# Optimization experiments

Measured on AMD Instinct MI355X. Metric: run time of the kernel, lower is better.

## Reference

```python
import jax, jax.numpy as jnp
import numpy as np

B, S, E, H, N, M, V = 8, 64, 64, 8, 2, 2, 50257
F = E  # outTrans FF hidden == embedding_size (4th ctor arg)


def setup_inputs() -> dict:
    key = jax.random.key(0)
    ks = jax.random.split(key, 10)
    sc = float(1.0 / np.sqrt(E))
    return {
        "noise": jax.random.uniform(ks[0], (B, S), jnp.float32),
        "lin_W": jax.random.normal(ks[1], (M, S, S), jnp.float32) * float(1.0 / np.sqrt(S)),
        "lin_b": jnp.zeros((M, S), jnp.float32),
        "sa_W": jax.random.normal(ks[2], (N, 4, E, E), jnp.float32) * sc,  # q,k,v,o
        "sa_b": jnp.zeros((N, 4, E), jnp.float32),
        "ca_W": jax.random.normal(ks[3], (N, 4, E, E), jnp.float32) * sc,
        "ca_b": jnp.zeros((N, 4, E), jnp.float32),
        "ff_W1": jax.random.normal(ks[4], (N, E, F), jnp.float32) * sc,
        "ff_b1": jnp.zeros((N, F), jnp.float32),
        "ff_W2": jax.random.normal(ks[5], (N, F, E), jnp.float32) * float(1.0 / np.sqrt(F)),
        "ff_b2": jnp.zeros((N, E), jnp.float32),
        "ln_g": jnp.ones((N, 3, E), jnp.float32),
        "ln_b": jnp.zeros((N, 3, E), jnp.float32),
        "emb": jax.random.normal(ks[6], (V, E), jnp.float32),
        "soft_W": jax.random.normal(ks[7], (E, V), jnp.float32) * sc,
        "soft_b": jnp.zeros((V,), jnp.float32),
        "start_id": 0,
    }


def _layernorm(x, g, b):
    m = jnp.mean(x, -1, keepdims=True)
    v = jnp.var(x, -1, keepdims=True)
    return (x - m) * jax.lax.rsqrt(v + 1e-5) * g + b


def _mha(qx, kvx, key_mask, W, bias):
    # W: [4,E,E] = (q,k,v,out). key_mask: [S] bool, True = valid key position.
    Bq, Sq, Eq = qx.shape
    d = Eq // H
    q = (qx @ W[0] + bias[0]).reshape(Bq, Sq, H, d)
    k = (kvx @ W[1] + bias[1]).reshape(Bq, -1, H, d)
    v = (kvx @ W[2] + bias[2]).reshape(Bq, -1, H, d)
    s = jnp.einsum('bqhd,bkhd->bhqk', q, k) / np.float32(np.sqrt(d))
    s = jnp.where(key_mask[None, None, None, :], s, jnp.float32(-1e9))
    a = jax.nn.softmax(s, axis=-1)
    o = jnp.einsum('bhqk,bkhd->bqhd', a, v).reshape(Bq, Sq, Eq)
    return o @ W[3] + bias[3]


def _pos_enc():
    pos = jnp.arange(S, dtype=jnp.float32)[:, None]
    i = jnp.arange(0, E, 2, dtype=jnp.float32)[None, :]
    ang = pos / jnp.power(jnp.float32(10000.0), i / E)
    pe = jnp.zeros((S, E), jnp.float32)
    return pe.at[:, 0::2].set(jnp.sin(ang)).at[:, 1::2].set(jnp.cos(ang))


def _forward(noise, lin_W, lin_b, sa_W, sa_b, ca_W, ca_b, ff_W1, ff_b1,
             ff_W2, ff_b2, ln_g, ln_b, emb, soft_W, soft_b, start_id):
    # inEmb2: M stacked Linear(S,S) on the noise
    w = noise
    for m in range(M):
        w = w @ lin_W[m] + lin_b[m]
    # unsqueeze(-1).repeat -> [B,S,S]; feature dim S == E
    w = jnp.repeat(w[:, :, None], S, axis=2)
    pe = _pos_enc()  # dropout p=0.1 is identity (module calls eval())
    Y0 = jnp.zeros((B, S, E), jnp.float32).at[:, 0].set(emb[start_id] + pe[0])

    def step(Y, tok):
        # Original re-runs all blocks on Y[:, :tok] each step (no KV cache).
        # We keep a fixed [B,S,E] buffer and mask keys >= tok: masked softmax
        # gives math identical to the truncated computation at valid positions.
        key_mask = jnp.arange(S) < tok
        out = Y
        for n in range(N):
            h = _mha(out, out, key_mask, sa_W[n], sa_b[n])
            out = _layernorm(out + h, ln_g[n, 0], ln_b[n, 0])
            h = _mha(out, w, key_mask, ca_W[n], ca_b[n])
            out = _layernorm(out + h, ln_g[n, 1], ln_b[n, 1])
            h = jax.nn.relu(out @ ff_W1[n] + ff_b1[n]) @ ff_W2[n] + ff_b2[n]
            out = _layernorm(out + h, ln_g[n, 2], ln_b[n, 2])
        tok_feat = out[:, tok - 1]                              # [B,E]
        probs = jax.nn.softmax(tok_feat @ soft_W + soft_b, -1)  # [B,V]
        nxt = jnp.argmax(probs, axis=-1)                        # greedy token
        Y = Y.at[:, tok].set(emb[nxt] + pe[tok])
        return Y, probs

    _, probs = jax.lax.scan(step, Y0, jnp.arange(1, S))
    return jnp.transpose(probs, (1, 0, 2))  # [B, S-1, V]


def reference(noise, lin_W, lin_b, sa_W, sa_b, ca_W, ca_b, ff_W1, ff_b1,
              ff_W2, ff_b2, ln_g, ln_b, emb, soft_W, soft_b, start_id):
    return _forward(noise, lin_W, lin_b, sa_W, sa_b, ca_W, ca_b, ff_W1, ff_b1,
                    ff_W2, ff_b2, ln_g, ln_b, emb, soft_W, soft_b, start_id)
```

## Files before the change

### kernel.cpp

```cpp
#include <hip/hip_runtime.h>
#include <math.h>

#define Vc 50257
#define NEG_INF (-__builtin_inff())
#define VCOLS 512
#define NVB 99
#define NB  8

#define WS_PE    0
#define WS_WV    4096
#define WS_CS    4608
#define WS_TOKF  4864
#define WS_MS    5376
#define WS_X2    5632
#define WS_SM    8192
#define WS_SS    9216
#define WS_SI    10240
#define WS_X1    16384
#define WS_Q1    49152
#define WS_K1    81920
#define WS_V1    114688
#define WS_K2G   147456
#define WS_V2G   180224


__device__ __forceinline__ float wsum64(float v) {
#pragma unroll
  for (int m = 32; m >= 1; m >>= 1) v += __shfl_xor(v, m, 64);
  return v;
}

__device__ __forceinline__ float red8(float v) {
  v += __shfl_xor(v, 1, 64);
  v += __shfl_xor(v, 2, 64);
  v += __shfl_xor(v, 4, 64);
  return v;
}

__device__ __forceinline__ float proj_lds(float xv, float* xb,
                                          const float* W,
                                          const float* __restrict__ bias, int lane) {
  xb[lane] = xv;
  asm volatile("s_waitcnt lgkmcnt(0)" ::: "memory");
  float acc = bias[lane];
  const float4* x4 = (const float4*)xb;
#pragma unroll
  for (int i = 0; i < 16; ++i) {
    float4 xc = x4[i];
    acc = fmaf(xc.x, W[(4 * i + 0) * 64 + lane], acc);
    acc = fmaf(xc.y, W[(4 * i + 1) * 64 + lane], acc);
    acc = fmaf(xc.z, W[(4 * i + 2) * 64 + lane], acc);
    acc = fmaf(xc.w, W[(4 * i + 3) * 64 + lane], acc);
  }
  asm volatile("" ::: "memory");
  return acc;
}

__device__ __forceinline__ float ln64(float xv, const float* __restrict__ g,
                                      const float* __restrict__ b, int lane) {
  float mean = wsum64(xv) * 0.015625f;
  float d = xv - mean;
  float var = wsum64(d * d) * 0.015625f;
  float r = 1.0f / sqrtf(var + 1e-5f);
  return d * r * g[lane] + b[lane];
}

struct LayerR {
  const float *saW3, *sab3, *caW0, *cab0, *caW3, *cab3,
              *ffW1, *ffb1, *ffW2, *ffb2, *g0, *be0, *g1, *be1, *g2, *be2;
  float cs1_r, cs2_r, cab1_r, cab2_r;
};

__device__ __forceinline__ void build_layer_s(LayerR& L, int n, int lane,
    const float* sWl, const float* sa_b, const float* ca_b,
    const float* ff_W1, const float* ff_b1, const float* ff_W2, const float* ff_b2,
    const float* ln_g, const float* ln_b, const float* cs_g) {
  L.saW3 = sWl;              L.sab3 = sa_b + (n * 4 + 3) * 64;
  L.caW0 = sWl + 4096;       L.cab0 = ca_b + (n * 4 + 0) * 64;
  L.caW3 = sWl + 2 * 4096;   L.cab3 = ca_b + (n * 4 + 3) * 64;
  L.ffW1 = ff_W1 + n * 4096; L.ffb1 = ff_b1 + n * 64;
  L.ffW2 = ff_W2 + n * 4096; L.ffb2 = ff_b2 + n * 64;
  L.g0 = ln_g + (n * 3 + 0) * 64;  L.be0 = ln_b + (n * 3 + 0) * 64;
  L.g1 = ln_g + (n * 3 + 1) * 64;  L.be1 = ln_b + (n * 3 + 1) * 64;
  L.g2 = ln_g + (n * 3 + 2) * 64;  L.be2 = ln_b + (n * 3 + 2) * 64;
  L.cab1_r = ca_b[(n * 4 + 1) * 64 + lane];
  L.cab2_r = ca_b[(n * 4 + 2) * 64 + lane];
  L.cs1_r = cs_g[(n * 2 + 0) * 64 + lane];
  L.cs2_r = cs_g[(n * 2 + 1) * 64 + lane];
}

__device__ float transformer_row(int lane, int t, float x, float q,
                                 const float* Kb, const float* Vb,
                                 const float* wv, float* xb, float* pb,
                                 const LayerR& P) {
  const float ISQ8 = 0.35355339059327373f;
  xb[lane] = q;
  asm volatile("s_waitcnt lgkmcnt(0)" ::: "memory");
  float a[8] = {0.f, 0.f, 0.f, 0.f, 0.f, 0.f, 0.f, 0.f};
  const float* Krow = Kb + lane * 65;
  const float4* xq4 = (const float4*)xb;
#pragma unroll
  for (int i = 0; i < 16; ++i) {
    float4 xc = xq4[i];
    a[i >> 1] = fmaf(xc.x, Krow[4 * i + 0], a[i >> 1]);
    a[i >> 1] = fmaf(xc.y, Krow[4 * i + 1], a[i >> 1]);
    a[i >> 1] = fmaf(xc.z, Krow[4 * i + 2], a[i >> 1]);
    a[i >> 1] = fmaf(xc.w, Krow[4 * i + 3], a[i >> 1]);
  }
  const bool act = lane < t;
  float m[8];
#pragma unroll
  for (int h = 0; h < 8; ++h) { a[h] = act ? a[h] * ISQ8 : NEG_INF; m[h] = a[h]; }
#pragma unroll
  for (int msk = 1; msk < 64; msk <<= 1) {
#pragma unroll
    for (int h = 0; h < 8; ++h) m[h] = fmaxf(m[h], __shfl_xor(m[h], msk, 64));
  }
  float l[8];
#pragma unroll
  for (int h = 0; h < 8; ++h) { a[h] = act ? expf(a[h] - m[h]) : 0.f; l[h] = a[h]; }
#pragma unroll
  for (int msk = 1; msk < 64; msk <<= 1) {
#pragma unroll
    for (int h = 0; h < 8; ++h) l[h] += __shfl_xor(l[h], msk, 64);
  }
#pragma unroll
  for (int h = 0; h < 8; ++h) pb[h * 64 + lane] = a[h] / l[h];
  asm volatile("s_waitcnt lgkmcnt(0)" ::: "memory");
  const float* pr = pb + (lane >> 3) * 64;
  float attn = 0.f;
  for (int k = 0; k < t; ++k) attn = fmaf(pr[k], Vb[k * 65 + lane], attn);

  float y1 = ln64(x + proj_lds(attn, xb, P.saW3, P.sab3, lane), P.g0, P.be0, lane);
  float qc = proj_lds(y1, xb, P.caW0, P.cab0, lane);
  float pa = red8(qc * P.cs1_r);
  float pc = red8(qc * P.cab1_r);
  const float4* wv4 = (const float4*)wv;
  float mc = NEG_INF;
#pragma unroll
  for (int i = 0; i < 16; ++i) {
    float4 wq = wv4[i];
    int k = 4 * i;
    if (k + 0 < t) mc = fmaxf(mc, fmaf(pa, wq.x, pc));
    if (k + 1 < t) mc = fmaxf(mc, fmaf(pa, wq.y, pc));
    if (k + 2 < t) mc = fmaxf(mc, fmaf(pa, wq.z, pc));
    if (k + 3 < t) mc = fmaxf(mc, fmaf(pa, wq.w, pc));
  }
  float lc = 0.f, z = 0.f;
#pragma unroll
  for (int i = 0; i < 16; ++i) {
    float4 wq = wv4[i];
    int k = 4 * i;
    float wk[4] = {wq.x, wq.y, wq.z, wq.w};
#pragma unroll
    for (int j = 0; j < 4; ++j) {
      if (k + j < t) {
        float raw = fmaf(pa, wk[j], pc);
        float pw = expf((raw - mc) * ISQ8);
        lc += pw;
        z = fmaf(pw, wk[j], z);
      }
    }
  }
  float oc = fmaf(z / lc, P.cs2_r, P.cab2_r);
  float y2 = ln64(y1 + proj_lds(oc, xb, P.caW3, P.cab3, lane), P.g1, P.be1, lane);
  float f = fmaxf(proj_lds(y2, xb, P.ffW1, P.ffb1, lane), 0.f);
  float y3 = ln64(y2 + proj_lds(f, xb, P.ffW2, P.ffb2, lane), P.g2, P.be2, lane);
  return y3;
}

__global__ __launch_bounds__(1024) void init_kernel(
    const float* __restrict__ noise, const float* __restrict__ lin_W,
    const float* __restrict__ lin_b, const float* __restrict__ sa_W,
    const float* __restrict__ sa_b, const float* __restrict__ ca_W,
    const float* __restrict__ emb, const int* __restrict__ start_id,
    float* __restrict__ wsf) {
  const int tid = threadIdx.x, lane = tid & 63, wvid = tid >> 6;
  __shared__ float xbuf[16 * 64];
  float* myxb = xbuf + wvid * 64;

  for (int i = tid; i < 62 * 64; i += 1024) {
    int t = 1 + (i >> 6), e = i & 63;
    double ang = (double)t / pow(10000.0, (double)(e & 62) / 64.0);
    wsf[WS_PE + t * 64 + e] = (e & 1) ? (float)cos(ang) : (float)sin(ang);
  }
  if (wvid < 8) {
    int b = wvid;
    float nz = noise[b * 64 + lane];
    float t1 = proj_lds(nz, myxb, lin_W, lin_b, lane);
    wsf[WS_WV + b * 64 + lane] = proj_lds(t1, myxb, lin_W + 4096, lin_b + 64, lane);
  } else if (wvid < 12) {
    int w = wvid - 8, n = w >> 1, which = w & 1;
    float c = 0.f;
    for (int e = 0; e < 64; ++e) c += ca_W[(n * 4 + 1 + which) * 4096 + e * 64 + lane];
    wsf[WS_CS + w * 64 + lane] = c;
  } else {
    for (int b = (wvid - 12) * 2; b <= (wvid - 12) * 2 + 1; ++b) {
      float y0 = emb[start_id[0] * 64 + lane] + ((lane & 1) ? 1.0f : 0.0f);
      float q0 = proj_lds(y0, myxb, sa_W, sa_b, lane);
      float k0 = proj_lds(y0, myxb, sa_W + 4096, sa_b + 64, lane);
      float v0 = proj_lds(y0, myxb, sa_W + 2 * 4096, sa_b + 128, lane);
      wsf[WS_X1 + b * 4096 + lane] = y0;
      wsf[WS_Q1 + b * 4096 + lane] = q0;
      wsf[WS_K1 + b * 4096 + lane] = k0;
      wsf[WS_V1 + b * 4096 + lane] = v0;
    }
  }
}

__global__ __launch_bounds__(1024) void l1_kernel(
    const float* __restrict__ sa_W, const float* __restrict__ sa_b,
    const float* __restrict__ ca_W, const float* __restrict__ ca_b,
    const float* __restrict__ ff_W1, const float* __restrict__ ff_b1,
    const float* __restrict__ ff_W2, const float* __restrict__ ff_b2,
    const float* __restrict__ ln_g, const float* __restrict__ ln_b,
    const float* __restrict__ emb, float* __restrict__ wsf, int t) {
  const int tid = threadIdx.x, lane = tid & 63, wvid = tid >> 6;
  const int b = blockIdx.x >> 2, sb = blockIdx.x & 3;
  __shared__ float lds[29888];
  float* sW   = lds;
  float* K1l  = lds + 12288;
  float* V1l  = lds + 16384;
  float* wvl  = lds + 20480;
  float* ynew = lds + 20544;
  float* qnew = lds + 20608;
  float* xbuf = lds + 20672;
  float* pbuf = lds + 21696;
  float* myxb = xbuf + wvid * 64;
  float* mypb = pbuf + wvid * 512;

  if (t <= 63) {
    float4* d = (float4*)sW;
    d[tid]        = ((const float4*)(sa_W + 3 * 4096))[tid];
    d[1024 + tid] = ((const float4*)(ca_W))[tid];
    d[2048 + tid] = ((const float4*)(ca_W + 3 * 4096))[tid];
    int upto = (t >= 2) ? t - 1 : t;
    for (int r = wvid; r < upto; r += 16) {
      K1l[r * 65 + lane] = wsf[WS_K1 + b * 4096 + r * 64 + lane];
      V1l[r * 65 + lane] = wsf[WS_V1 + b * 4096 + r * 64 + lane];
    }
    if (wvid == 1) wvl[lane] = wsf[WS_WV + b * 64 + lane];
  }

  if (t >= 2 && wvid == 0) {
    const float* smp = wsf + WS_SM + b * 128;
    const float* ssp = wsf + WS_SS + b * 128;
    const int*   sip = (const int*)(wsf + WS_SI) + b * 128;
    float mA = smp[lane];
    float sA = ssp[lane];
    int   iA = sip[lane];
    const bool a2 = (64 + lane) < NVB;
    float mB = a2 ? smp[64 + lane] : NEG_INF;
    float sB = a2 ? ssp[64 + lane] : 0.f;
    int   iB = a2 ? sip[64 + lane] : 0x7fffffff;
    float mg = mA; int ig = iA;
    if (mB > mg || (mB == mg && iB < ig)) { mg = mB; ig = iB; }
#pragma unroll
    for (int msk = 1; msk < 64; msk <<= 1) {
      float om = __shfl_xor(mg, msk, 64);
      int oi = __shfl_xor(ig, msk, 64);
      if (om > mg || (om == mg && oi < ig)) { mg = om; ig = oi; }
    }
    float part = sA * expf(mA - mg) + (a2 ? sB * expf(mB - mg) : 0.f);
    float S = wsum64(part);
    if (lane == 0) { wsf[WS_MS + b * 2] = mg; wsf[WS_MS + b * 2 + 1] = S; }
    if (t <= 63) {
      float y = emb[ig * 64 + lane] + wsf[WS_PE + (t - 1) * 64 + lane];
      float qn = proj_lds(y, myxb, sa_W, sa_b, lane);
      float kn = proj_lds(y, myxb, sa_W + 4096, sa_b + 64, lane);
      float vn = proj_lds(y, myxb, sa_W + 2 * 4096, sa_b + 128, lane);
      K1l[(t - 1) * 65 + lane] = kn;
      V1l[(t - 1) * 65 + lane] = vn;
      ynew[lane] = y; qnew[lane] = qn;
      if (sb == ((t - 1) >> 4)) {
        wsf[WS_X1 + b * 4096 + (t - 1) * 64 + lane] = y;
        wsf[WS_Q1 + b * 4096 + (t - 1) * 64 + lane] = qn;
        wsf[WS_K1 + b * 4096 + (t - 1) * 64 + lane] = kn;
        wsf[WS_V1 + b * 4096 + (t - 1) * 64 + lane] = vn;
      }
    }
  }
  __syncthreads();
  if (t > 63) return;

  const int row = sb * 16 + wvid;
  if (row < t) {
    float x_r, q_r;
    if (t >= 2 && row == t - 1) { x_r = ynew[lane]; q_r = qnew[lane]; }
    else {
      x_r = wsf[WS_X1 + b * 4096 + row * 64 + lane];
      q_r = wsf[WS_Q1 + b * 4096 + row * 64 + lane];
    }
    LayerR L0;
    build_layer_s(L0, 0, lane, sW, sa_b, ca_b, ff_W1, ff_b1, ff_W2, ff_b2,
                  ln_g, ln_b, wsf + WS_CS);
    float out = transformer_row(lane, t, x_r, q_r, K1l, V1l, wvl, myxb, mypb, L0);
    float k2 = proj_lds(out, myxb, sa_W + 5 * 4096, sa_b + 5 * 64, lane);
    float v2 = proj_lds(out, myxb, sa_W + 6 * 4096, sa_b + 6 * 64, lane);
    wsf[WS_K2G + b * 4096 + row * 64 + lane] = k2;
    wsf[WS_V2G + b * 4096 + row * 64 + lane] = v2;
    if (row == t - 1) wsf[WS_X2 + b * 64 + lane] = out;
  }
}

__global__ __launch_bounds__(1024) void l2_kernel(
    const float* __restrict__ sa_W, const float* __restrict__ sa_b,
    const float* __restrict__ ca_W, const float* __restrict__ ca_b,
    const float* __restrict__ ff_W1, const float* __restrict__ ff_b1,
    const float* __restrict__ ff_W2, const float* __restrict__ ff_b2,
    const float* __restrict__ ln_g, const float* __restrict__ ln_b,
    float* __restrict__ wsf, int t) {
  const int tid = threadIdx.x, lane = tid & 63, wvid = tid >> 6;
  const int b = blockIdx.x;
  __shared__ float lds[22592];
  float* sW   = lds;
  float* K2l  = lds + 12288;
  float* V2l  = lds + 16384;
  float* wvl  = lds + 20480;
  float* xbuf = lds + 20544;
  float* pbuf = lds + 21568;
  float* myxb = xbuf + wvid * 64;

  float4* d = (float4*)sW;
  d[tid]        = ((const float4*)(sa_W + 7 * 4096))[tid];
  d[1024 + tid] = ((const float4*)(ca_W + 4 * 4096))[tid];
  d[2048 + tid] = ((const float4*)(ca_W + 7 * 4096))[tid];
  for (int r = wvid; r < t; r += 16) {
    K2l[r * 65 + lane] = wsf[WS_K2G + b * 4096 + r * 64 + lane];
    V2l[r * 65 + lane] = wsf[WS_V2G + b * 4096 + r * 64 + lane];
  }
  if (wvid == 1) wvl[lane] = wsf[WS_WV + b * 64 + lane];
  __syncthreads();

  if (wvid == 0) {
    LayerR L1;
    build_layer_s(L1, 1, lane, sW, sa_b, ca_b, ff_W1, ff_b1, ff_W2, ff_b2,
                  ln_g, ln_b, wsf + WS_CS);
    float x2 = wsf[WS_X2 + b * 64 + lane];
    float q2 = proj_lds(x2, myxb, sa_W + 4 * 4096, sa_b + 4 * 64, lane);
    float tf = transformer_row(lane, t, x2, q2, K2l, V2l, wvl, myxb, pbuf, L1);
    wsf[WS_TOKF + b * 64 + lane] = tf;
  }
}

__global__ __launch_bounds__(512) void vocab_kernel(
    const float* __restrict__ soft_W, const float* __restrict__ soft_b,
    float* __restrict__ wsf, float* __restrict__ dout, int t) {
  const int tid = threadIdx.x, lane = tid & 63, wvid = tid >> 6;
  const int jb = blockIdx.x;
  const int v = jb * VCOLS + tid;
  const bool valid = v < Vc;
  __shared__ float f2[512];
  __shared__ float sm[64];  __shared__ int si[64];
  __shared__ float ssm[64];
  __shared__ float bmx[8];  __shared__ int bix[8];

  if (t >= 2 && valid) {
    long row = (long)(t - 2) * Vc + v;
#pragma unroll
    for (int b2 = 0; b2 < 8; ++b2) {
      float m = wsf[WS_MS + b2 * 2], S = wsf[WS_MS + b2 * 2 + 1];
      long idx = (long)b2 * 63 * Vc + row;
      dout[idx] = expf(dout[idx] - m) / S;
    }
  }
  if (t > 63) return;

  f2[tid] = wsf[WS_TOKF + (tid & 7) * 64 + (tid >> 3)];
  __syncthreads();
  float sb = valid ? soft_b[v] : 0.f;
  float lg[8];
#pragma unroll
  for (int b = 0; b < 8; ++b) lg[b] = valid ? sb : NEG_INF;
  if (valid) {
    const float4* f4 = (const float4*)f2;
    const float* col = soft_W + v;
#pragma unroll 8
    for (int e = 0; e < 64; ++e) {
      float wc = col[(long)e * Vc];
      float4 fa = f4[2 * e], fb = f4[2 * e + 1];
      lg[0] = fmaf(fa.x, wc, lg[0]);
      lg[1] = fmaf(fa.y, wc, lg[1]);
      lg[2] = fmaf(fa.z, wc, lg[2]);
      lg[3] = fmaf(fa.w, wc, lg[3]);
      lg[4] = fmaf(fb.x, wc, lg[4]);
      lg[5] = fmaf(fb.y, wc, lg[5]);
      lg[6] = fmaf(fb.z, wc, lg[6]);
      lg[7] = fmaf(fb.w, wc, lg[7]);
    }
  }
#pragma unroll
  for (int b = 0; b < 8; ++b) {
    float m = lg[b]; int ix = valid ? v : 0x7fffffff;
#pragma unroll
    for (int msk = 1; msk < 64; msk <<= 1) {
      float om = __shfl_xor(m, msk, 64);
      int oi = __shfl_xor(ix, msk, 64);
      if (om > m || (om == m && oi < ix)) { m = om; ix = oi; }
    }
    if (lane == 0) { sm[wvid * 8 + b] = m; si[wvid * 8 + b] = ix; }
  }
  __syncthreads();
  if (tid < 8) {
    float m = NEG_INF; int ix = 0x7fffffff;
    for (int wv = 0; wv < 8; ++wv) {
      float om = sm[wv * 8 + tid]; int oi = si[wv * 8 + tid];
      if (om > m || (om == m && oi < ix)) { m = om; ix = oi; }
    }
    bmx[tid] = m; bix[tid] = ix;
  }
  __syncthreads();
#pragma unroll
  for (int b = 0; b < 8; ++b) {
    float c = valid ? expf(lg[b] - bmx[b]) : 0.f;
    float s = wsum64(c);
    if (lane == 0) ssm[wvid * 8 + b] = s;
  }
  __syncthreads();
  if (tid < 8) {
    float s = 0.f;
    for (int wv = 0; wv < 8; ++wv) s += ssm[wv * 8 + tid];
    wsf[WS_SM + tid * 128 + jb] = bmx[tid];
    wsf[WS_SS + tid * 128 + jb] = s;
    ((int*)(wsf + WS_SI))[tid * 128 + jb] = bix[tid];
  }
  if (valid) {
    long row = (long)(t - 1) * Vc + v;
#pragma unroll
    for (int b = 0; b < 8; ++b) dout[(long)b * 63 * Vc + row] = lg[b];
  }
}

extern "C" void kernel_launch(void* const* d_in, const int* in_sizes, int n_in,
                              void* d_out, int out_size, void* d_ws, size_t ws_size,
                              hipStream_t stream) {
  (void)in_sizes; (void)n_in; (void)out_size; (void)ws_size;
  const float* noise  = (const float*)d_in[0];
  const float* lin_W  = (const float*)d_in[1];
  const float* lin_b  = (const float*)d_in[2];
  const float* sa_W   = (const float*)d_in[3];
  const float* sa_b   = (const float*)d_in[4];
  const float* ca_W   = (const float*)d_in[5];
  const float* ca_b   = (const float*)d_in[6];
  const float* ff_W1  = (const float*)d_in[7];
  const float* ff_b1  = (const float*)d_in[8];
  const float* ff_W2  = (const float*)d_in[9];
  const float* ff_b2  = (const float*)d_in[10];
  const float* ln_g   = (const float*)d_in[11];
  const float* ln_b   = (const float*)d_in[12];
  const float* emb    = (const float*)d_in[13];
  const float* soft_W = (const float*)d_in[14];
  const float* soft_b = (const float*)d_in[15];
  const int*   start  = (const int*)d_in[16];
  float* dout = (float*)d_out;
  float* wsf  = (float*)d_ws;

  init_kernel<<<1, 1024, 0, stream>>>(noise, lin_W, lin_b, sa_W, sa_b, ca_W,
                                      emb, start, wsf);
  for (int t = 1; t <= 63; ++t) {
    l1_kernel<<<32, 1024, 0, stream>>>(sa_W, sa_b, ca_W, ca_b, ff_W1, ff_b1,
                                       ff_W2, ff_b2, ln_g, ln_b, emb, wsf, t);
    l2_kernel<<<NB, 1024, 0, stream>>>(sa_W, sa_b, ca_W, ca_b, ff_W1, ff_b1,
                                       ff_W2, ff_b2, ln_g, ln_b, wsf, t);
    vocab_kernel<<<NVB, 512, 0, stream>>>(soft_W, soft_b, wsf, dout, t);
  }
  l1_kernel<<<32, 1024, 0, stream>>>(sa_W, sa_b, ca_W, ca_b, ff_W1, ff_b1,
                                     ff_W2, ff_b2, ln_g, ln_b, emb, wsf, 64);
  vocab_kernel<<<NVB, 512, 0, stream>>>(soft_W, soft_b, wsf, dout, 64);
}
```

Measured before the change: 3.986 ms.

## Fuse layer-2 last-token transformer into vocab kernel, parallelize positional-encoding init

Removes the separate l2_kernel launch per decode step. Instead, every vocab block redundantly recomputes the layer-2 transformer row for all 8 batches, one wave per batch, reading K/V and weights directly from global memory. The result goes into shared memory and feeds the logits. It also spreads the positional-encoding table computation over 63 init blocks. This saves one launch and one global round trip per step, at the cost of 99-fold redundant layer-2 compute with unstaged global loads inside the vocab kernel.

```diff
diff --git a/kernel.cpp b/kernel.cpp
--- a/kernel.cpp
+++ b/kernel.cpp
@@ -10,7 +10,6 @@
 #define WS_PE    0
 #define WS_WV    4096
 #define WS_CS    4608
-#define WS_TOKF  4864
 #define WS_MS    5376
 #define WS_X2    5632
 #define WS_SM    8192
@@ -89,15 +88,33 @@
   L.cs2_r = cs_g[(n * 2 + 1) * 64 + lane];
 }
 
+__device__ __forceinline__ void build_layer_g(LayerR& L, int n, int lane,
+    const float* sa_W, const float* sa_b, const float* ca_W, const float* ca_b,
+    const float* ff_W1, const float* ff_b1, const float* ff_W2, const float* ff_b2,
+    const float* ln_g, const float* ln_b, const float* cs_g) {
+  L.saW3 = sa_W + (n * 4 + 3) * 4096; L.sab3 = sa_b + (n * 4 + 3) * 64;
+  L.caW0 = ca_W + (n * 4 + 0) * 4096; L.cab0 = ca_b + (n * 4 + 0) * 64;
+  L.caW3 = ca_W + (n * 4 + 3) * 4096; L.cab3 = ca_b + (n * 4 + 3) * 64;
+  L.ffW1 = ff_W1 + n * 4096;          L.ffb1 = ff_b1 + n * 64;
+  L.ffW2 = ff_W2 + n * 4096;          L.ffb2 = ff_b2 + n * 64;
+  L.g0 = ln_g + (n * 3 + 0) * 64;     L.be0 = ln_b + (n * 3 + 0) * 64;
+  L.g1 = ln_g + (n * 3 + 1) * 64;     L.be1 = ln_b + (n * 3 + 1) * 64;
+  L.g2 = ln_g + (n * 3 + 2) * 64;     L.be2 = ln_b + (n * 3 + 2) * 64;
+  L.cab1_r = ca_b[(n * 4 + 1) * 64 + lane];
+  L.cab2_r = ca_b[(n * 4 + 2) * 64 + lane];
+  L.cs1_r = cs_g[(n * 2 + 0) * 64 + lane];
+  L.cs2_r = cs_g[(n * 2 + 1) * 64 + lane];
+}
+
 __device__ float transformer_row(int lane, int t, float x, float q,
-                                 const float* Kb, const float* Vb,
+                                 const float* Kb, const float* Vb, int ks,
                                  const float* wv, float* xb, float* pb,
                                  const LayerR& P) {
   const float ISQ8 = 0.35355339059327373f;
   xb[lane] = q;
   asm volatile("s_waitcnt lgkmcnt(0)" ::: "memory");
   float a[8] = {0.f, 0.f, 0.f, 0.f, 0.f, 0.f, 0.f, 0.f};
-  const float* Krow = Kb + lane * 65;
+  const float* Krow = Kb + lane * ks;
   const float4* xq4 = (const float4*)xb;
 #pragma unroll
   for (int i = 0; i < 16; ++i) {
@@ -129,7 +146,7 @@
   asm volatile("s_waitcnt lgkmcnt(0)" ::: "memory");
   const float* pr = pb + (lane >> 3) * 64;
   float attn = 0.f;
-  for (int k = 0; k < t; ++k) attn = fmaf(pr[k], Vb[k * 65 + lane], attn);
+  for (int k = 0; k < t; ++k) attn = fmaf(pr[k], Vb[k * ks + lane], attn);
 
   float y1 = ln64(x + proj_lds(attn, xb, P.saW3, P.sab3, lane), P.g0, P.be0, lane);
   float qc = proj_lds(y1, xb, P.caW0, P.cab0, lane);
@@ -176,13 +193,17 @@
     const float* __restrict__ emb, const int* __restrict__ start_id,
     float* __restrict__ wsf) {
   const int tid = threadIdx.x, lane = tid & 63, wvid = tid >> 6;
+  const int blk = blockIdx.x;
   __shared__ float xbuf[16 * 64];
   float* myxb = xbuf + wvid * 64;
 
-  for (int i = tid; i < 62 * 64; i += 1024) {
-    int t = 1 + (i >> 6), e = i & 63;
-    double ang = (double)t / pow(10000.0, (double)(e & 62) / 64.0);
-    wsf[WS_PE + t * 64 + e] = (e & 1) ? (float)cos(ang) : (float)sin(ang);
+  if (blk > 0) {
+    if (tid < 64) {
+      int t = blk, e = tid;
+      double ang = (double)t / pow(10000.0, (double)(e & 62) / 64.0);
+      wsf[WS_PE + t * 64 + e] = (e & 1) ? (float)cos(ang) : (float)sin(ang);
+    }
+    return;
   }
   if (wvid < 8) {
     int b = wvid;
@@ -294,7 +315,7 @@
     LayerR L0;
     build_layer_s(L0, 0, lane, sW, sa_b, ca_b, ff_W1, ff_b1, ff_W2, ff_b2,
                   ln_g, ln_b, wsf + WS_CS);
-    float out = transformer_row(lane, t, x_r, q_r, K1l, V1l, wvl, myxb, mypb, L0);
+    float out = transformer_row(lane, t, x_r, q_r, K1l, V1l, 65, wvl, myxb, mypb, L0);
     float k2 = proj_lds(out, myxb, sa_W + 5 * 4096, sa_b + 5 * 64, lane);
     float v2 = proj_lds(out, myxb, sa_W + 6 * 4096, sa_b + 6 * 64, lane);
     wsf[WS_K2G + b * 4096 + row * 64 + lane] = k2;
@@ -303,54 +324,22 @@
   }
 }
 
-__global__ __launch_bounds__(1024) void l2_kernel(
+__global__ __launch_bounds__(512) void vocab_kernel(
     const float* __restrict__ sa_W, const float* __restrict__ sa_b,
     const float* __restrict__ ca_W, const float* __restrict__ ca_b,
     const float* __restrict__ ff_W1, const float* __restrict__ ff_b1,
     const float* __restrict__ ff_W2, const float* __restrict__ ff_b2,
     const float* __restrict__ ln_g, const float* __restrict__ ln_b,
-    float* __restrict__ wsf, int t) {
-  const int tid = threadIdx.x, lane = tid & 63, wvid = tid >> 6;
-  const int b = blockIdx.x;
-  __shared__ float lds[22592];
-  float* sW   = lds;
-  float* K2l  = lds + 12288;
-  float* V2l  = lds + 16384;
-  float* wvl  = lds + 20480;
-  float* xbuf = lds + 20544;
-  float* pbuf = lds + 21568;
-  float* myxb = xbuf + wvid * 64;
-
-  float4* d = (float4*)sW;
-  d[tid]        = ((const float4*)(sa_W + 7 * 4096))[tid];
-  d[1024 + tid] = ((const float4*)(ca_W + 4 * 4096))[tid];
-  d[2048 + tid] = ((const float4*)(ca_W + 7 * 4096))[tid];
-  for (int r = wvid; r < t; r += 16) {
-    K2l[r * 65 + lane] = wsf[WS_K2G + b * 4096 + r * 64 + lane];
-    V2l[r * 65 + lane] = wsf[WS_V2G + b * 4096 + r * 64 + lane];
-  }
-  if (wvid == 1) wvl[lane] = wsf[WS_WV + b * 64 + lane];
-  __syncthreads();
-
-  if (wvid == 0) {
-    LayerR L1;
-    build_layer_s(L1, 1, lane, sW, sa_b, ca_b, ff_W1, ff_b1, ff_W2, ff_b2,
-                  ln_g, ln_b, wsf + WS_CS);
-    float x2 = wsf[WS_X2 + b * 64 + lane];
-    float q2 = proj_lds(x2, myxb, sa_W + 4 * 4096, sa_b + 4 * 64, lane);
-    float tf = transformer_row(lane, t, x2, q2, K2l, V2l, wvl, myxb, pbuf, L1);
-    wsf[WS_TOKF + b * 64 + lane] = tf;
-  }
-}
-
-__global__ __launch_bounds__(512) void vocab_kernel(
     const float* __restrict__ soft_W, const float* __restrict__ soft_b,
     float* __restrict__ wsf, float* __restrict__ dout, int t) {
   const int tid = threadIdx.x, lane = tid & 63, wvid = tid >> 6;
   const int jb = blockIdx.x;
   const int v = jb * VCOLS + tid;
   const bool valid = v < Vc;
+  __shared__ float tokf_l[512];
   __shared__ float f2[512];
+  __shared__ float xb8[512];
+  __shared__ float pb8[4096];
   __shared__ float sm[64];  __shared__ int si[64];
   __shared__ float ssm[64];
   __shared__ float bmx[8];  __shared__ int bix[8];
@@ -366,7 +355,23 @@
   }
   if (t > 63) return;
 
-  f2[tid] = wsf[WS_TOKF + (tid & 7) * 64 + (tid >> 3)];
+  {
+    const int b2 = wvid;
+    float* myxb = xb8 + wvid * 64;
+    float* mypb = pb8 + wvid * 512;
+    LayerR L1;
+    build_layer_g(L1, 1, lane, sa_W, sa_b, ca_W, ca_b, ff_W1, ff_b1, ff_W2, ff_b2,
+                  ln_g, ln_b, wsf + WS_CS);
+    float x2 = wsf[WS_X2 + b2 * 64 + lane];
+    float q2 = proj_lds(x2, myxb, sa_W + 4 * 4096, sa_b + 4 * 64, lane);
+    float tf = transformer_row(lane, t, x2, q2,
+                               wsf + WS_K2G + b2 * 4096, wsf + WS_V2G + b2 * 4096, 64,
+                               wsf + WS_WV + b2 * 64, myxb, mypb, L1);
+    tokf_l[b2 * 64 + lane] = tf;
+  }
+  __syncthreads();
+
+  f2[tid] = tokf_l[(tid & 7) * 64 + (tid >> 3)];
   __syncthreads();
   float sb = valid ? soft_b[v] : 0.f;
   float lg[8];
@@ -455,16 +460,18 @@
   float* dout = (float*)d_out;
   float* wsf  = (float*)d_ws;
 
-  init_kernel<<<1, 1024, 0, stream>>>(noise, lin_W, lin_b, sa_W, sa_b, ca_W,
-                                      emb, start, wsf);
+  init_kernel<<<63, 1024, 0, stream>>>(noise, lin_W, lin_b, sa_W, sa_b, ca_W,
+                                       emb, start, wsf);
   for (int t = 1; t <= 63; ++t) {
     l1_kernel<<<32, 1024, 0, stream>>>(sa_W, sa_b, ca_W, ca_b, ff_W1, ff_b1,
                                        ff_W2, ff_b2, ln_g, ln_b, emb, wsf, t);
-    l2_kernel<<<NB, 1024, 0, stream>>>(sa_W, sa_b, ca_W, ca_b, ff_W1, ff_b1,
-                                       ff_W2, ff_b2, ln_g, ln_b, wsf, t);
-    vocab_kernel<<<NVB, 512, 0, stream>>>(soft_W, soft_b, wsf, dout, t);
+    vocab_kernel<<<NVB, 512, 0, stream>>>(sa_W, sa_b, ca_W, ca_b, ff_W1, ff_b1,
+                                          ff_W2, ff_b2, ln_g, ln_b,
+                                          soft_W, soft_b, wsf, dout, t);
   }
   l1_kernel<<<32, 1024, 0, stream>>>(sa_W, sa_b, ca_W, ca_b, ff_W1, ff_b1,
                                      ff_W2, ff_b2, ln_g, ln_b, emb, wsf, 64);
-  vocab_kernel<<<NVB, 512, 0, stream>>>(soft_W, soft_b, wsf, dout, 64);
-}
+  vocab_kernel<<<NVB, 512, 0, stream>>>(sa_W, sa_b, ca_W, ca_b, ff_W1, ff_b1,
+                                        ff_W2, ff_b2, ln_g, ln_b,
+                                        soft_W, soft_b, wsf, dout, 64);
+}
```

Measured after the change: 4.161 ms. 4.4% more time.
